# Optimization experiments

Hardware: AMD Instinct MI355X
Metric: run time of the kernel (lower is better)

The kernel has to match this reference:

```python
import jax, jax.numpy as jnp
import numpy as np

B, S, DIN, H, DOUT, E, SEL = 8, 2048, 512, 512, 512, 262144, 512
N = B * S


def setup_inputs() -> dict:
    key = jax.random.key(0)
    ks = jax.random.split(key, 20)
    inp = {
        "x": jax.random.normal(ks[0], (B, S, DIN), dtype=jnp.float32),
        "edge_index": jax.random.randint(ks[1], (2, E), 0, N, dtype=jnp.int64),
        "selected_idx": jax.random.randint(ks[2], (B, SEL), 0, S, dtype=jnp.int64),
        "edge_label": jax.random.randint(ks[3], (E,), 0, 8, dtype=jnp.int64),
    }
    k = 4
    for l, fin in enumerate([DIN, H, H]):
        inp[f"conv{l}_w1"] = jax.random.normal(ks[k], (2 * fin, H), dtype=jnp.float32) * 0.02; k += 1
        inp[f"conv{l}_b1"] = jnp.full((H,), 0.01, dtype=jnp.float32)
        inp[f"conv{l}_w2"] = jax.random.normal(ks[k], (H, H), dtype=jnp.float32) * 0.02; k += 1
        inp[f"conv{l}_b2"] = jnp.full((H,), 0.01, dtype=jnp.float32)
    inp["ffn_w1"] = jax.random.normal(ks[k], (H, H), dtype=jnp.float32) * 0.02; k += 1
    inp["ffn_b1"] = jnp.full((H,), 0.01, dtype=jnp.float32)
    inp["ffn_w2"] = jax.random.normal(ks[k], (H, DOUT), dtype=jnp.float32) * 0.02; k += 1
    inp["ffn_b2"] = jnp.full((DOUT,), 0.01, dtype=jnp.float32)
    return inp


def _ffw(x, w1, b1, w2, b2):
    # FeedForward: fc2(act_dropout(relu(fc1(x)))), dropout=0 in eval
    return jax.nn.relu(x @ w1 + b1) @ w2 + b2


def reference(x, edge_index, selected_idx, edge_label,
              conv0_w1, conv0_b1, conv0_w2, conv0_b2,
              conv1_w1, conv1_b1, conv1_w2, conv1_b2,
              conv2_w1, conv2_b1, conv2_w2, conv2_b2,
              ffn_w1, ffn_b1, ffn_w2, ffn_b2):
    b, s, d = x.shape
    n = b * s
    h = x.reshape(n, d)
    src, dst = edge_index[0], edge_index[1]  # PyG: x_j = source, x_i = target
    convs = [(conv0_w1, conv0_b1, conv0_w2, conv0_b2),
             (conv1_w1, conv1_b1, conv1_w2, conv1_b2),
             (conv2_w1, conv2_b1, conv2_w2, conv2_b2)]
    for w1, b1, w2, b2 in convs:
        xi = h[dst]                                   # [E, F]
        xj = h[src]
        ef = jnp.concatenate([xi, xj - xi], axis=1)   # [E, 2F]
        m = _ffw(ef, w1, b1, w2, b2)                  # per-edge MLP [E, H]
        agg = jax.ops.segment_max(m, dst, num_segments=n)
        agg = jnp.where(jnp.isneginf(agg), 0.0, agg)  # empty segments -> 0 (PyG fill)
        h = jax.nn.relu(agg)                          # dropout p acts as identity in eval
    h = _ffw(h, ffn_w1, ffn_b1, ffn_w2, ffn_b2)
    out = h.reshape(b, s, -1)                         # [B, S, DOUT]
    idx = jnp.broadcast_to(selected_idx[:, :, None], (b, selected_idx.shape[1], out.shape[-1]))
    return jnp.take_along_axis(out, idx, axis=1)      # [B, SEL, DOUT]
```

## Files before the change

### kernel.cpp

```cpp
#include <hip/hip_runtime.h>
#include <hip/hip_bf16.h>


#define N_NODES 16384
#define EDGES   262144
#define HDIM    512
#define SEQ     2048

typedef __attribute__((ext_vector_type(8))) short short8;
typedef __attribute__((ext_vector_type(8))) _Float16 half8;
typedef __attribute__((ext_vector_type(2))) _Float16 half2v;
typedef __attribute__((ext_vector_type(4))) float f32x4;

__device__ __forceinline__ void gld16(const void* g, void* l) {
    __builtin_amdgcn_global_load_lds(
        (const __attribute__((address_space(1))) void*)g,
        (__attribute__((address_space(3))) void*)l, 16, 0, 0);
}
__device__ __forceinline__ unsigned short f2b(float f) {
    unsigned int x = __float_as_uint(f);
    return (unsigned short)((x + 0x7fffu + ((x >> 16) & 1u)) >> 16);
}
__device__ __forceinline__ unsigned short f2h(float f) {
    _Float16 h = (_Float16)f;
    return __builtin_bit_cast(unsigned short, h);
}
__device__ __forceinline__ unsigned int zpack_h(unsigned int u, unsigned int v) {
    half2v a = __builtin_bit_cast(half2v, u);
    half2v b = __builtin_bit_cast(half2v, v);
    half2v s = a + b;
    half2v z = {(_Float16)0.f, (_Float16)0.f};
    half2v r = __builtin_elementwise_max(s, z);
    return __builtin_bit_cast(unsigned int, r);
}
__device__ __forceinline__ short8 frag_ld(const short* S, int row, int q) {
    int p = q ^ ((row >> 1) & 3);
    return *(const short8*)(S + row * 32 + p * 8);
}
__device__ __forceinline__ void stage_tile(const short* G, int kc, short* S, int t) {
#pragma unroll
    for (int it = 0; it < 2; ++it) {
        int lin = it * 256 + t;
        int row = lin >> 2, p = lin & 3;
        int q = p ^ ((row >> 1) & 3);
        gld16(G + (size_t)row * HDIM + kc + q * 8, S + lin * 8);
    }
}
__device__ __forceinline__ half8 frag64(const short* S, int row, int q) {
    int p = q ^ ((row >> 1) & 7) ^ (row & 1);
    return *(const half8*)(S + row * 64 + p * 8);
}
__device__ __forceinline__ void stageB32(const short* __restrict__ Wt, int n0, int col0,
                                         short* buf, int t) {
#pragma unroll
    for (int it = 0; it < 4; ++it) {
        int lin = it * 256 + t;
        int row = lin >> 2, s = lin & 3;
        int q = s ^ ((row >> 1) & 3);
        gld16(Wt + (size_t)(n0 + row) * HDIM + col0 + q * 8, buf + lin * 8);
    }
}

__global__ __launch_bounds__(256) void hist_kernel(
    const int* __restrict__ dst, int* __restrict__ hist) {
    int idx = blockIdx.x * 256 + threadIdx.x;
    atomicAdd(&hist[dst[idx]], 1);
}
__global__ __launch_bounds__(256) void scan_kernel(
    const int* __restrict__ hist, int* __restrict__ cursor) {
    __shared__ int part[256];
    const int t = threadIdx.x, base = t * 64;
    int sum = 0;
    for (int i = 0; i < 64; ++i) sum += hist[base + i];
    part[t] = sum;
    __syncthreads();
    int run = 0;
    for (int i = 0; i < t; ++i) run += part[i];
    for (int i = 0; i < 64; ++i) {
        int h = hist[base + i];
        cursor[base + i] = run;
        run += h;
    }
}
__global__ __launch_bounds__(256) void scatter_kernel(
    const int* __restrict__ dst, const int* __restrict__ src,
    int* __restrict__ cursor, int* __restrict__ dstS, int* __restrict__ srcS) {
    int idx = blockIdx.x * 256 + threadIdx.x;
    int d = dst[idx];
    int p = atomicAdd(&cursor[d], 1);
    dstS[p] = d;
    srcS[p] = src[idx];
}

__global__ __launch_bounds__(256) void prep_weights_all_kernel(
    const float* __restrict__ w1_0, const float* __restrict__ w2_0,
    const float* __restrict__ w1_1, const float* __restrict__ w2_1,
    const float* __restrict__ w1_2, const float* __restrict__ w2_2,
    short* __restrict__ outbase) {
    __shared__ float tile[32][33];
    const int z = blockIdx.z;
    const int layer = z / 3, which = z % 3;
    const float* w1 = layer == 0 ? w1_0 : (layer == 1 ? w1_1 : w1_2);
    const float* w2 = layer == 0 ? w2_0 : (layer == 1 ? w2_1 : w2_2);
    const int k0 = blockIdx.x * 32, n0 = blockIdx.y * 32;
    const int tx = threadIdx.x, ty = threadIdx.y;
#pragma unroll
    for (int i = 0; i < 4; ++i) {
        int k = k0 + ty + i * 8, n = n0 + tx;
        float v;
        if (which == 0)      v = w1[k * 512 + n] - w1[(k + 512) * 512 + n];
        else if (which == 1) v = w1[(k + 512) * 512 + n];
        else                 v = w2[k * 512 + n];
        tile[ty + i * 8][tx] = v;
    }
    __syncthreads();
    short* out = outbase + (size_t)(layer * 3 + which) * 512 * 512;
#pragma unroll
    for (int i = 0; i < 4; ++i) {
        int n = n0 + ty + i * 8, k = k0 + tx;
        float v = tile[tx][ty + i * 8];
        out[(size_t)n * 512 + k] = (short)(which == 2 ? f2h(v) : f2b(v));
    }
}
__global__ __launch_bounds__(256) void tr_kernel(
    const float* __restrict__ W1, const float* __restrict__ W2,
    short* __restrict__ T1, short* __restrict__ T2) {
    __shared__ float tile[32][33];
    const float* W = blockIdx.z ? W2 : W1;
    short* T = blockIdx.z ? T2 : T1;
    const int k0 = blockIdx.x * 32, n0 = blockIdx.y * 32;
    const int tx = threadIdx.x, ty = threadIdx.y;
#pragma unroll
    for (int i = 0; i < 4; ++i)
        tile[ty + i * 8][tx] = W[(k0 + ty + i * 8) * 512 + n0 + tx];
    __syncthreads();
#pragma unroll
    for (int i = 0; i < 4; ++i)
        T[(size_t)(n0 + ty + i * 8) * 512 + k0 + tx] = (short)f2b(tile[tx][ty + i * 8]);
}
__global__ __launch_bounds__(256) void cvt_bf16_kernel(
    const float* __restrict__ x, short* __restrict__ xb) {
    int idx = blockIdx.x * 256 + threadIdx.x;
    float4 v = ((const float4*)x)[idx];
    uint2 o;
    o.x = (unsigned int)f2b(v.x) | ((unsigned int)f2b(v.y) << 16);
    o.y = (unsigned int)f2b(v.z) | ((unsigned int)f2b(v.w) << 16);
    ((uint2*)xb)[idx] = o;
}

__global__ __launch_bounds__(256, 2) void node_gemm_uv_kernel(
    const short* __restrict__ A, const short* __restrict__ WdT,
    const short* __restrict__ w1bT, const float* __restrict__ b1,
    short* __restrict__ U, short* __restrict__ V) {
    __shared__ short As[2][128 * 32];
    __shared__ short Bu[2][128 * 32];
    __shared__ short Bv[2][128 * 32];
    const int t = threadIdx.x;
    const int m0 = blockIdx.x * 128, n0 = blockIdx.y * 128;
    const int w = t >> 6, l = t & 63;
    const int wm = (w & 1) * 64, wn = (w >> 1) * 64;
    const short* Ag = A + (size_t)m0 * HDIM;
    const short* Ug = WdT + (size_t)n0 * HDIM;
    const short* Vg = w1bT + (size_t)n0 * HDIM;
    f32x4 aU[4][4] = {}, aV[4][4] = {};
    stage_tile(Ag, 0, As[0], t);
    stage_tile(Ug, 0, Bu[0], t);
    stage_tile(Vg, 0, Bv[0], t);
#pragma unroll
    for (int hh = 0; hh < 16; ++hh) {
        if (hh < 15) {
            const int kc1 = (hh + 1) * 32;
            stage_tile(Ag, kc1, As[(hh + 1) & 1], t);
            stage_tile(Ug, kc1, Bu[(hh + 1) & 1], t);
            stage_tile(Vg, kc1, Bv[(hh + 1) & 1], t);
            asm volatile("s_waitcnt vmcnt(6)" ::: "memory");
        } else {
            asm volatile("s_waitcnt vmcnt(0)" ::: "memory");
        }
        __builtin_amdgcn_s_barrier();
        asm volatile("" ::: "memory");
        const short* Ab = As[hh & 1];
        const short* Bub = Bu[hh & 1];
        const short* Bvb = Bv[hh & 1];
        short8 a[4], bu[4], bv[4];
#pragma unroll
        for (int mt = 0; mt < 4; ++mt) a[mt] = frag_ld(Ab, wm + mt * 16 + (l & 15), l >> 4);
#pragma unroll
        for (int nt = 0; nt < 4; ++nt) {
            bu[nt] = frag_ld(Bub, wn + nt * 16 + (l & 15), l >> 4);
            bv[nt] = frag_ld(Bvb, wn + nt * 16 + (l & 15), l >> 4);
        }
#pragma unroll
        for (int mt = 0; mt < 4; ++mt)
#pragma unroll
            for (int nt = 0; nt < 4; ++nt) {
                aU[mt][nt] = __builtin_amdgcn_mfma_f32_16x16x32_bf16(a[mt], bu[nt], aU[mt][nt], 0, 0, 0);
                aV[mt][nt] = __builtin_amdgcn_mfma_f32_16x16x32_bf16(a[mt], bv[nt], aV[mt][nt], 0, 0, 0);
            }
        asm volatile("" ::: "memory");
        __builtin_amdgcn_s_barrier();
    }
#pragma unroll
    for (int mt = 0; mt < 4; ++mt) {
        int m = m0 + wm + mt * 16 + (l >> 4) * 4;
#pragma unroll
        for (int nt = 0; nt < 4; ++nt) {
            int n = n0 + wn + nt * 16 + (l & 15);
            float bv = b1[n];
#pragma unroll
            for (int r = 0; r < 4; ++r) {
                U[(size_t)(m + r) * HDIM + n] = (short)f2h(aU[mt][nt][r] + bv);
                V[(size_t)(m + r) * HDIM + n] = (short)f2h(aV[mt][nt][r]);
            }
        }
    }
}

__device__ __forceinline__ unsigned int fkey(float m) {
    unsigned int b = __float_as_uint(m);
    return ((int)b < 0) ? ~b : (b | 0x80000000u);
}
__device__ __forceinline__ void kflush(unsigned int* K, int d, int col, float m) {
    atomicMax(K + (((size_t)d) << 9) + col, fkey(m));
}
__global__ __launch_bounds__(256, 3) void edge_mfma_kernel(
    const short* __restrict__ U, const short* __restrict__ V,
    const short* __restrict__ Wt, const int* __restrict__ srcS,
    const int* __restrict__ dstS, unsigned int* __restrict__ K) {
    __shared__ short As[64 * 64];
    __shared__ short Bs[2][256 * 32];
    __shared__ int sdst[64], ssrc[64];
    const int t = threadIdx.x;
    const int L  = blockIdx.x;
    const int g  = (L >> 4) * 8 + (L & 7);
    const int nh = (L >> 3) & 1;
    const int e0 = g * 64, n0 = nh * 256;
    if (t < 64) { sdst[t] = dstS[e0 + t]; ssrc[t] = srcS[e0 + t]; }
    __syncthreads();
    const int w = t >> 6, l = t & 63;
    const int wnb = w * 64;
    const int lm = l & 15;
    const int arow = t >> 2, s0 = (t & 3) * 2;
    const int perm = ((arow >> 1) & 7) ^ (arow & 1);
    const int p0 = s0 ^ perm, p1 = (s0 + 1) ^ perm;
    const short* up = U + (((size_t)sdst[arow]) << 9) + s0 * 8;
    const short* vp = V + (((size_t)ssrc[arow]) << 9) + s0 * 8;
    unsigned int* As_u = (unsigned int*)As;
    f32x4 acc[4][4] = {};
    uint4 pu0, pu1, pv0, pv1, nu0, nu1, nv0, nv1;
    stageB32(Wt, n0, 0, Bs[0], t);
    pu0 = *(const uint4*)(up);
    pu1 = *(const uint4*)(up + 8);
    pv0 = *(const uint4*)(vp);
    pv1 = *(const uint4*)(vp + 8);
#pragma unroll
    for (int hh = 0; hh < 16; ++hh) {
        const int kc = (hh >> 1) * 64;
        if (hh < 15) {
            const int c1 = ((hh + 1) >> 1) * 64 + ((hh + 1) & 1) * 32;
            stageB32(Wt, n0, c1, Bs[(hh + 1) & 1], t);
        }
        if ((hh & 1) == 0) {
            if (hh < 14) {
                nu0 = *(const uint4*)(up + kc + 64);
                nu1 = *(const uint4*)(up + kc + 64 + 8);
                nv0 = *(const uint4*)(vp + kc + 64);
                nv1 = *(const uint4*)(vp + kc + 64 + 8);
            }
            uint4 z0, z1;
            z0.x = zpack_h(pu0.x, pv0.x); z0.y = zpack_h(pu0.y, pv0.y);
            z0.z = zpack_h(pu0.z, pv0.z); z0.w = zpack_h(pu0.w, pv0.w);
            z1.x = zpack_h(pu1.x, pv1.x); z1.y = zpack_h(pu1.y, pv1.y);
            z1.z = zpack_h(pu1.z, pv1.z); z1.w = zpack_h(pu1.w, pv1.w);
            *(uint4*)(As_u + arow * 32 + p0 * 4) = z0;
            *(uint4*)(As_u + arow * 32 + p1 * 4) = z1;
        }
        if (hh < 14)       asm volatile("s_waitcnt vmcnt(8) lgkmcnt(0)" ::: "memory");
        else if (hh == 14) asm volatile("s_waitcnt vmcnt(4) lgkmcnt(0)" ::: "memory");
        else               asm volatile("s_waitcnt vmcnt(0) lgkmcnt(0)" ::: "memory");
        __builtin_amdgcn_s_barrier();
        asm volatile("" ::: "memory");
        const short* Bb = Bs[hh & 1];
        const int hq = (hh & 1) * 4 + (l >> 4);
        __builtin_amdgcn_s_setprio(1);
        half8 b[4];
#pragma unroll
        for (int nt = 0; nt < 4; ++nt) {
            int row = wnb + nt * 16 + lm;
            int p = (l >> 4) ^ ((row >> 1) & 3);
            b[nt] = *(const half8*)(Bb + row * 32 + p * 8);
        }
#pragma unroll
        for (int mt = 0; mt < 4; ++mt) {
            half8 a = frag64(As, mt * 16 + lm, hq);
#pragma unroll
            for (int nt = 0; nt < 4; ++nt)
                acc[mt][nt] = __builtin_amdgcn_mfma_f32_16x16x32_f16(a, b[nt], acc[mt][nt], 0, 0, 0);
        }
        __builtin_amdgcn_s_setprio(0);
        if ((hh & 1) == 0 && hh < 14) { pu0 = nu0; pu1 = nu1; pv0 = nv0; pv1 = nv1; }
        asm volatile("" ::: "memory");
        __builtin_amdgcn_s_barrier();
    }
    const int dbase = sdst[0];
    const int drange = sdst[63] - dbase + 1;
    unsigned int* tile = (unsigned int*)Bs[1];
    if (drange <= 16) {
#pragma unroll
        for (int i = 0; i < 16; ++i) tile[i * 256 + t] = 0u;
        __syncthreads();
#pragma unroll
        for (int mt = 0; mt < 4; ++mt) {
            int base = mt * 16 + (l >> 4) * 4;
            int d0 = sdst[base], d1 = sdst[base + 1], d2 = sdst[base + 2], d3 = sdst[base + 3];
            int r0 = d0 - dbase, r1 = d1 - dbase, r2 = d2 - dbase, r3 = d3 - dbase;
#pragma unroll
            for (int nt = 0; nt < 4; ++nt) {
                int colb = wnb + nt * 16 + lm;
                f32x4 a = acc[mt][nt];
                float m = a[0];
                if (d1 == d0) m = fmaxf(m, a[1]);
                else { atomicMax(tile + r0 * 256 + colb, fkey(m)); m = a[1]; }
                if (d2 == d1) m = fmaxf(m, a[2]);
                else { atomicMax(tile + r1 * 256 + colb, fkey(m)); m = a[2]; }
                if (d3 == d2) m = fmaxf(m, a[3]);
                else { atomicMax(tile + r2 * 256 + colb, fkey(m)); m = a[3]; }
                atomicMax(tile + r3 * 256 + colb, fkey(m));
            }
        }
        __syncthreads();
#pragma unroll 4
        for (int r = 0; r < 16; ++r) {
            if (r < drange) {
                unsigned int kv = tile[r * 256 + t];
                if (kv) atomicMax(K + (((size_t)(dbase + r)) << 9) + n0 + t, kv);
            }
        }
    } else {
#pragma unroll
        for (int mt = 0; mt < 4; ++mt) {
            int base = mt * 16 + (l >> 4) * 4;
            int d0 = sdst[base], d1 = sdst[base + 1], d2 = sdst[base + 2], d3 = sdst[base + 3];
#pragma unroll
            for (int nt = 0; nt < 4; ++nt) {
                int col = n0 + wnb + nt * 16 + lm;
                f32x4 a = acc[mt][nt];
                float m = a[0];
                if (d1 == d0) m = fmaxf(m, a[1]); else { kflush(K, d0, col, m); m = a[1]; }
                if (d2 == d1) m = fmaxf(m, a[2]); else { kflush(K, d1, col, m); m = a[2]; }
                if (d3 == d2) m = fmaxf(m, a[3]); else { kflush(K, d2, col, m); m = a[3]; }
                kflush(K, d3, col, m);
            }
        }
    }
}

__global__ __launch_bounds__(256) void decode_kernel(
    unsigned int* __restrict__ K, const float* __restrict__ b2,
    short* __restrict__ hb) {
    int idx = blockIdx.x * 256 + threadIdx.x;
    uint2 k = ((uint2*)K)[idx];
    uint2 zz = {0u, 0u};
    ((uint2*)K)[idx] = zz;
    int c = (idx << 1) & (HDIM - 1);
    float v0 = 0.f, v1 = 0.f;
    if (k.x != 0u) {
        unsigned int b = (k.x & 0x80000000u) ? (k.x ^ 0x80000000u) : ~k.x;
        v0 = __uint_as_float(b) + b2[c];
    }
    if (k.y != 0u) {
        unsigned int b = (k.y & 0x80000000u) ? (k.y ^ 0x80000000u) : ~k.y;
        v1 = __uint_as_float(b) + b2[c + 1];
    }
    unsigned int o = (unsigned int)f2b(fmaxf(v0, 0.f))
                   | ((unsigned int)f2b(fmaxf(v1, 0.f)) << 16);
    ((unsigned int*)hb)[idx] = o;
}

__global__ __launch_bounds__(256) void ffn_gemm_kernel(
    const short* __restrict__ A, const int* __restrict__ sel,
    const short* __restrict__ Wt, const float* __restrict__ bias,
    short* __restrict__ Cb, float* __restrict__ Cf, int relu) {
    __shared__ short As[64 * 32];
    __shared__ short Bs[128 * 32];
    const int t = threadIdx.x;
    const int m0 = blockIdx.x * 64, n0 = blockIdx.y * 128;
    const int w = t >> 6, l = t & 63;
    const int wm = (w & 1) * 32, wn = (w >> 1) * 64;
    const int srow = t >> 2, sp = t & 3;
    const int sq = sp ^ ((srow >> 1) & 3);
    const short* ap;
    if (sel) {
        int gr = m0 + srow;
        ap = A + (((size_t)((gr >> 9) * SEQ + sel[gr])) << 9);
    } else {
        ap = A + (size_t)(m0 + srow) * HDIM;
    }
    f32x4 acc[2][4] = {};
    for (int kc = 0; kc < HDIM; kc += 32) {
        gld16(ap + kc + sq * 8, As + t * 8);
        stage_tile(Wt + (size_t)n0 * HDIM, kc, Bs, t);
        __syncthreads();
        short8 a[2], b[4];
#pragma unroll
        for (int mt = 0; mt < 2; ++mt) a[mt] = frag_ld(As, wm + mt * 16 + (l & 15), l >> 4);
#pragma unroll
        for (int nt = 0; nt < 4; ++nt) b[nt] = frag_ld(Bs, wn + nt * 16 + (l & 15), l >> 4);
#pragma unroll
        for (int mt = 0; mt < 2; ++mt)
#pragma unroll
            for (int nt = 0; nt < 4; ++nt)
                acc[mt][nt] = __builtin_amdgcn_mfma_f32_16x16x32_bf16(a[mt], b[nt], acc[mt][nt], 0, 0, 0);
        __syncthreads();
    }
#pragma unroll
    for (int mt = 0; mt < 2; ++mt) {
        int m = m0 + wm + mt * 16 + (l >> 4) * 4;
#pragma unroll
        for (int nt = 0; nt < 4; ++nt) {
            int n = n0 + wn + nt * 16 + (l & 15);
            float bv = bias[n];
#pragma unroll
            for (int r = 0; r < 4; ++r) {
                float v = acc[mt][nt][r] + bv;
                if (relu) v = fmaxf(v, 0.f);
                if (Cf) Cf[(size_t)(m + r) * HDIM + n] = v;
                else    Cb[(size_t)(m + r) * HDIM + n] = (short)f2b(v);
            }
        }
    }
}

extern "C" void kernel_launch(void* const* d_in, const int* in_sizes, int n_in,
                              void* d_out, int out_size, void* d_ws, size_t ws_size,
                              hipStream_t stream) {
    const float* x   = (const float*)d_in[0];
    const int*   ei  = (const int*)d_in[1];
    const int*   sel = (const int*)d_in[2];
    const int*   src = ei;
    const int*   dst = ei + EDGES;
    const float* cw1[3] = {(const float*)d_in[4],  (const float*)d_in[8],  (const float*)d_in[12]};
    const float* cb1[3] = {(const float*)d_in[5],  (const float*)d_in[9],  (const float*)d_in[13]};
    const float* cw2[3] = {(const float*)d_in[6],  (const float*)d_in[10], (const float*)d_in[14]};
    const float* cb2[3] = {(const float*)d_in[7],  (const float*)d_in[11], (const float*)d_in[15]};
    const float* fw1 = (const float*)d_in[16];
    const float* fb1 = (const float*)d_in[17];
    const float* fw2 = (const float*)d_in[18];
    const float* fb2 = (const float*)d_in[19];
    float* out = (float*)d_out;

    const size_t MB = 1024 * 1024;
    char* p = (char*)d_ws;
    unsigned int* keys = (unsigned int*)p;
    short* U    = (short*)(p + 32 * MB);
    short* V    = (short*)(p + 48 * MB);
    short* hb   = (short*)(p + 64 * MB);
    short* Wall = (short*)(p + 80 * MB);
    short* fw1T = Wall + 9 * 512 * 512;
    short* fw2T = fw1T + 512 * 512;
    int*   dstS = (int*)(p + 86 * MB);
    int*   srcS = (int*)(p + 87 * MB);
    int*   hist = (int*)(p + 88 * MB);
    int*   curs = hist + N_NODES;
    short* t1b  = (short*)(p + 89 * MB);

    (void)hipMemsetAsync(hist, 0, N_NODES * sizeof(int), stream);
    hist_kernel<<<EDGES / 256, 256, 0, stream>>>(dst, hist);
    scan_kernel<<<1, 256, 0, stream>>>(hist, curs);
    scatter_kernel<<<EDGES / 256, 256, 0, stream>>>(dst, src, curs, dstS, srcS);

    cvt_bf16_kernel<<<8192, 256, 0, stream>>>(x, hb);
    tr_kernel<<<dim3(16, 16, 2), dim3(32, 8), 0, stream>>>(fw1, fw2, fw1T, fw2T);
    prep_weights_all_kernel<<<dim3(16, 16, 9), dim3(32, 8), 0, stream>>>(
        cw1[0], cw2[0], cw1[1], cw2[1], cw1[2], cw2[2], Wall);
    (void)hipMemsetAsync(keys, 0, 32 * MB, stream);

    for (int l = 0; l < 3; ++l) {
        short* WdT  = Wall + (size_t)(l * 3 + 0) * 512 * 512;
        short* w1bT = Wall + (size_t)(l * 3 + 1) * 512 * 512;
        short* W2T  = Wall + (size_t)(l * 3 + 2) * 512 * 512;
        node_gemm_uv_kernel<<<dim3(128, 4), 256, 0, stream>>>(hb, WdT, w1bT, cb1[l], U, V);
        edge_mfma_kernel<<<8192, 256, 0, stream>>>(U, V, W2T, srcS, dstS, keys);
        decode_kernel<<<(N_NODES * HDIM / 2) / 256, 256, 0, stream>>>(keys, cb2[l], hb);
    }

    ffn_gemm_kernel<<<dim3(64, 4), 256, 0, stream>>>(hb, sel, fw1T, fb1, t1b, nullptr, 1);
    ffn_gemm_kernel<<<dim3(64, 4), 256, 0, stream>>>(t1b, nullptr, fw2T, fb2, nullptr, out, 0);
}
```

Baseline: 828.5 us.

## Load edge-MLP weight fragments directly into registers instead of LDS staging

The edge MFMA kernel no longer stages the Wt tile through double-buffered shared memory with async global-to-LDS loads. Each lane now reads its B fragments straight from global memory into registers, prefetching one 32-column half ahead. The A tile is rebuilt once per 64-column chunk, with two barriers per chunk. This frees LDS for higher occupancy and removes B staging traffic, but puts uncoalesced-ish per-lane weight reads on the critical path and relies on L2/L1 hits for Wt.

```diff
diff --git a/kernel.cpp b/kernel.cpp
--- a/kernel.cpp
+++ b/kernel.cpp
@@ -49,16 +49,6 @@
 __device__ __forceinline__ half8 frag64(const short* S, int row, int q) {
     int p = q ^ ((row >> 1) & 7) ^ (row & 1);
     return *(const half8*)(S + row * 64 + p * 8);
-}
-__device__ __forceinline__ void stageB32(const short* __restrict__ Wt, int n0, int col0,
-                                         short* buf, int t) {
-#pragma unroll
-    for (int it = 0; it < 4; ++it) {
-        int lin = it * 256 + t;
-        int row = lin >> 2, s = lin & 3;
-        int q = s ^ ((row >> 1) & 3);
-        gld16(Wt + (size_t)(n0 + row) * HDIM + col0 + q * 8, buf + lin * 8);
-    }
 }
 
 __global__ __launch_bounds__(256) void hist_kernel(
@@ -228,7 +218,7 @@
     const short* __restrict__ Wt, const int* __restrict__ srcS,
     const int* __restrict__ dstS, unsigned int* __restrict__ K) {
     __shared__ short As[64 * 64];
-    __shared__ short Bs[2][256 * 32];
+    __shared__ unsigned int ktile[16 * 256];
     __shared__ int sdst[64], ssrc[64];
     const int t = threadIdx.x;
     const int L  = blockIdx.x;
@@ -245,28 +235,62 @@
     const int p0 = s0 ^ perm, p1 = (s0 + 1) ^ perm;
     const short* up = U + (((size_t)sdst[arow]) << 9) + s0 * 8;
     const short* vp = V + (((size_t)ssrc[arow]) << 9) + s0 * 8;
+    const short* bp = Wt + (size_t)(n0 + wnb + lm) * HDIM + (l >> 4) * 8;
     unsigned int* As_u = (unsigned int*)As;
     f32x4 acc[4][4] = {};
-    uint4 pu0, pu1, pv0, pv1, nu0, nu1, nv0, nv1;
-    stageB32(Wt, n0, 0, Bs[0], t);
-    pu0 = *(const uint4*)(up);
-    pu1 = *(const uint4*)(up + 8);
-    pv0 = *(const uint4*)(vp);
-    pv1 = *(const uint4*)(vp + 8);
-#pragma unroll
-    for (int hh = 0; hh < 16; ++hh) {
-        const int kc = (hh >> 1) * 64;
-        if (hh < 15) {
-            const int c1 = ((hh + 1) >> 1) * 64 + ((hh + 1) & 1) * 32;
-            stageB32(Wt, n0, c1, Bs[(hh + 1) & 1], t);
-        }
-        if ((hh & 1) == 0) {
-            if (hh < 14) {
-                nu0 = *(const uint4*)(up + kc + 64);
-                nu1 = *(const uint4*)(up + kc + 64 + 8);
-                nv0 = *(const uint4*)(vp + kc + 64);
-                nv1 = *(const uint4*)(vp + kc + 64 + 8);
-            }
+    half8 bc[4], bn[4];
+    uint4 pu0, pu1, pv0, pv1;
+#pragma unroll
+    for (int nt = 0; nt < 4; ++nt) bc[nt] = *(const half8*)(bp + nt * 16 * HDIM);
+    pu0 = *(const uint4*)(up);      pu1 = *(const uint4*)(up + 8);
+    pv0 = *(const uint4*)(vp);      pv1 = *(const uint4*)(vp + 8);
+    {
+        uint4 z0, z1;
+        z0.x = zpack_h(pu0.x, pv0.x); z0.y = zpack_h(pu0.y, pv0.y);
+        z0.z = zpack_h(pu0.z, pv0.z); z0.w = zpack_h(pu0.w, pv0.w);
+        z1.x = zpack_h(pu1.x, pv1.x); z1.y = zpack_h(pu1.y, pv1.y);
+        z1.z = zpack_h(pu1.z, pv1.z); z1.w = zpack_h(pu1.w, pv1.w);
+        *(uint4*)(As_u + arow * 32 + p0 * 4) = z0;
+        *(uint4*)(As_u + arow * 32 + p1 * 4) = z1;
+    }
+    pu0 = *(const uint4*)(up + 64); pu1 = *(const uint4*)(up + 72);
+    pv0 = *(const uint4*)(vp + 64); pv1 = *(const uint4*)(vp + 72);
+    asm volatile("s_waitcnt lgkmcnt(0)" ::: "memory");
+    __builtin_amdgcn_s_barrier();
+    asm volatile("" ::: "memory");
+#pragma unroll
+    for (int j = 0; j < 8; ++j) {
+        const int h1 = 2 * j + 1;
+#pragma unroll
+        for (int nt = 0; nt < 4; ++nt)
+            bn[nt] = *(const half8*)(bp + nt * 16 * HDIM + h1 * 32);
+        __builtin_amdgcn_s_setprio(1);
+#pragma unroll
+        for (int mt = 0; mt < 4; ++mt) {
+            half8 a = frag64(As, mt * 16 + lm, (l >> 4));
+#pragma unroll
+            for (int nt = 0; nt < 4; ++nt)
+                acc[mt][nt] = __builtin_amdgcn_mfma_f32_16x16x32_f16(a, bc[nt], acc[mt][nt], 0, 0, 0);
+        }
+        __builtin_amdgcn_s_setprio(0);
+        if (j < 7) {
+#pragma unroll
+            for (int nt = 0; nt < 4; ++nt)
+                bc[nt] = *(const half8*)(bp + nt * 16 * HDIM + (h1 + 1) * 32);
+        }
+        __builtin_amdgcn_s_setprio(1);
+#pragma unroll
+        for (int mt = 0; mt < 4; ++mt) {
+            half8 a = frag64(As, mt * 16 + lm, 4 + (l >> 4));
+#pragma unroll
+            for (int nt = 0; nt < 4; ++nt)
+                acc[mt][nt] = __builtin_amdgcn_mfma_f32_16x16x32_f16(a, bn[nt], acc[mt][nt], 0, 0, 0);
+        }
+        __builtin_amdgcn_s_setprio(0);
+        asm volatile("s_waitcnt lgkmcnt(0)" ::: "memory");
+        __builtin_amdgcn_s_barrier();
+        asm volatile("" ::: "memory");
+        if (j < 7) {
             uint4 z0, z1;
             z0.x = zpack_h(pu0.x, pv0.x); z0.y = zpack_h(pu0.y, pv0.y);
             z0.z = zpack_h(pu0.z, pv0.z); z0.w = zpack_h(pu0.w, pv0.w);
@@ -274,40 +298,21 @@
             z1.z = zpack_h(pu1.z, pv1.z); z1.w = zpack_h(pu1.w, pv1.w);
             *(uint4*)(As_u + arow * 32 + p0 * 4) = z0;
             *(uint4*)(As_u + arow * 32 + p1 * 4) = z1;
-        }
-        if (hh < 14)       asm volatile("s_waitcnt vmcnt(8) lgkmcnt(0)" ::: "memory");
-        else if (hh == 14) asm volatile("s_waitcnt vmcnt(4) lgkmcnt(0)" ::: "memory");
-        else               asm volatile("s_waitcnt vmcnt(0) lgkmcnt(0)" ::: "memory");
-        __builtin_amdgcn_s_barrier();
-        asm volatile("" ::: "memory");
-        const short* Bb = Bs[hh & 1];
-        const int hq = (hh & 1) * 4 + (l >> 4);
-        __builtin_amdgcn_s_setprio(1);
-        half8 b[4];
-#pragma unroll
-        for (int nt = 0; nt < 4; ++nt) {
-            int row = wnb + nt * 16 + lm;
-            int p = (l >> 4) ^ ((row >> 1) & 3);
-            b[nt] = *(const half8*)(Bb + row * 32 + p * 8);
-        }
-#pragma unroll
-        for (int mt = 0; mt < 4; ++mt) {
-            half8 a = frag64(As, mt * 16 + lm, hq);
-#pragma unroll
-            for (int nt = 0; nt < 4; ++nt)
-                acc[mt][nt] = __builtin_amdgcn_mfma_f32_16x16x32_f16(a, b[nt], acc[mt][nt], 0, 0, 0);
-        }
-        __builtin_amdgcn_s_setprio(0);
-        if ((hh & 1) == 0 && hh < 14) { pu0 = nu0; pu1 = nu1; pv0 = nv0; pv1 = nv1; }
-        asm volatile("" ::: "memory");
-        __builtin_amdgcn_s_barrier();
+            if (j < 6) {
+                const int kn = (j + 2) * 64;
+                pu0 = *(const uint4*)(up + kn);      pu1 = *(const uint4*)(up + kn + 8);
+                pv0 = *(const uint4*)(vp + kn);      pv1 = *(const uint4*)(vp + kn + 8);
+            }
+            asm volatile("s_waitcnt lgkmcnt(0)" ::: "memory");
+            __builtin_amdgcn_s_barrier();
+            asm volatile("" ::: "memory");
+        }
     }
     const int dbase = sdst[0];
     const int drange = sdst[63] - dbase + 1;
-    unsigned int* tile = (unsigned int*)Bs[1];
     if (drange <= 16) {
 #pragma unroll
-        for (int i = 0; i < 16; ++i) tile[i * 256 + t] = 0u;
+        for (int i = 0; i < 16; ++i) ktile[i * 256 + t] = 0u;
         __syncthreads();
 #pragma unroll
         for (int mt = 0; mt < 4; ++mt) {
@@ -320,19 +325,19 @@
                 f32x4 a = acc[mt][nt];
                 float m = a[0];
                 if (d1 == d0) m = fmaxf(m, a[1]);
-                else { atomicMax(tile + r0 * 256 + colb, fkey(m)); m = a[1]; }
+                else { atomicMax(ktile + r0 * 256 + colb, fkey(m)); m = a[1]; }
                 if (d2 == d1) m = fmaxf(m, a[2]);
-                else { atomicMax(tile + r1 * 256 + colb, fkey(m)); m = a[2]; }
+                else { atomicMax(ktile + r1 * 256 + colb, fkey(m)); m = a[2]; }
                 if (d3 == d2) m = fmaxf(m, a[3]);
-                else { atomicMax(tile + r2 * 256 + colb, fkey(m)); m = a[3]; }
-                atomicMax(tile + r3 * 256 + colb, fkey(m));
+                else { atomicMax(ktile + r2 * 256 + colb, fkey(m)); m = a[3]; }
+                atomicMax(ktile + r3 * 256 + colb, fkey(m));
             }
         }
         __syncthreads();
 #pragma unroll 4
         for (int r = 0; r < 16; ++r) {
             if (r < drange) {
-                unsigned int kv = tile[r * 256 + t];
+                unsigned int kv = ktile[r * 256 + t];
                 if (kv) atomicMax(K + (((size_t)(dbase + r)) << 9) + n0 + t, kv);
             }
         }
```

Result: slower. 1.083 ms (+30.7%).
